# Kernel tuning notes

Measured on AMD Instinct MI355X. Metric: run time of the kernel, lower is better.

The kernel has to match this reference:

```python
import jax, jax.numpy as jnp
import numpy as np

D = 1024
B, S = 4, 2048


def setup_inputs() -> dict:
    key = jax.random.key(0)
    ks = jax.random.split(key, 6)
    sc = 1.0 / np.sqrt(D)  # truncated-normal-ish fan-in scale like hk.Linear default
    return {
        "x": jax.random.normal(ks[0], (B, S, D), dtype=jnp.float32),
        "W_amp1": jax.random.normal(ks[1], (D, D), dtype=jnp.float32) * sc,
        "b_amp1": jnp.zeros((D,), dtype=jnp.float32),
        "W_amp2": jax.random.normal(ks[2], (D, D), dtype=jnp.float32) * sc,
        "b_amp2": jnp.zeros((D,), dtype=jnp.float32),
        "vqc_params": jax.random.uniform(ks[3], (D, 4), dtype=jnp.float32, minval=-np.pi, maxval=np.pi),
        "W_post1": jax.random.normal(ks[4], (D, D), dtype=jnp.float32) * sc,
        "b_post1": jnp.zeros((D,), dtype=jnp.float32),
        "W_post2": jax.random.normal(ks[5], (D, D), dtype=jnp.float32) * sc,
        "b_post2": jnp.zeros((D,), dtype=jnp.float32),
    }


def reference(x, W_amp1, b_amp1, W_amp2, b_amp2, vqc_params,
              W_post1, b_post1, W_post2, b_post2):
    # amplitude encoder: Linear -> tanh -> Linear
    amp = jnp.tanh(x @ W_amp1 + b_amp1) @ W_amp2 + b_amp2  # [B,S,D]

    # variational quantum circuit, vectorized over channels:
    # per-channel i: out_i = amp_i*cos(theta_i/2) + Re(amp_i*sin(theta_i/2)*e^{i phi_i})
    #              = amp_i * (cos(theta_i/2) + sin(theta_i/2)*cos(phi_i))
    theta = vqc_params[:, 0]  # [D]
    phi = vqc_params[:, 1]    # [D]
    scale = jnp.cos(theta * 0.5) + jnp.sin(theta * 0.5) * jnp.cos(phi)  # [D]
    q = amp * scale  # broadcast over [B,S,D]

    # classical post: Linear -> silu -> Linear
    out = jax.nn.silu(q @ W_post1 + b_post1) @ W_post2 + b_post2
    return out
```

## Files before the change

kernel.cpp:

```cpp
#include <hip/hip_runtime.h>
#include <hip/hip_bf16.h>
#include <math.h>

#define DD 1024
#define MM 8192

typedef __attribute__((ext_vector_type(8))) short short8;
typedef __attribute__((ext_vector_type(4))) float f32x4;

__device__ inline unsigned short f32_to_bf16(float f) {
  union { float f; unsigned u; } v; v.f = f;
  unsigned u = v.u;
  u += 0x7FFFu + ((u >> 16) & 1u);
  return (unsigned short)(u >> 16);
}

__global__ void k_convert_x(const float4* __restrict__ x, ushort4* __restrict__ o, int n4) {
  int i = blockIdx.x * blockDim.x + threadIdx.x;
  int stride = gridDim.x * blockDim.x;
  for (; i < n4; i += stride) {
    float4 v = x[i];
    ushort4 r;
    r.x = f32_to_bf16(v.x); r.y = f32_to_bf16(v.y);
    r.z = f32_to_bf16(v.z); r.w = f32_to_bf16(v.w);
    o[i] = r;
  }
}

__global__ void k_transpose_w(const float* __restrict__ w0, const float* __restrict__ w1,
                              const float* __restrict__ w2, const float* __restrict__ w3,
                              unsigned short* __restrict__ o0, unsigned short* __restrict__ o1,
                              unsigned short* __restrict__ o2, unsigned short* __restrict__ o3) {
  const float* src; unsigned short* dst;
  switch (blockIdx.z) {
    case 0: src = w0; dst = o0; break;
    case 1: src = w1; dst = o1; break;
    case 2: src = w2; dst = o2; break;
    default: src = w3; dst = o3; break;
  }
  __shared__ float t[32][33];
  int tx = threadIdx.x, ty = threadIdx.y;
  int c0 = blockIdx.x * 32, r0 = blockIdx.y * 32;
  #pragma unroll
  for (int i = 0; i < 4; i++)
    t[ty + 8 * i][tx] = src[(size_t)(r0 + ty + 8 * i) * DD + c0 + tx];
  __syncthreads();
  #pragma unroll
  for (int i = 0; i < 4; i++)
    dst[(size_t)(c0 + ty + 8 * i) * DD + r0 + tx] = f32_to_bf16(t[tx][ty + 8 * i]);
}

__global__ void k_scale(const float* __restrict__ vqc, float* __restrict__ sc) {
  int d = blockIdx.x * blockDim.x + threadIdx.x;
  if (d < DD) {
    float th = vqc[d * 4 + 0] * 0.5f, ph = vqc[d * 4 + 1];
    sc[d] = cosf(th) + sinf(th) * cosf(ph);
  }
}

template <int EPI>
__global__ void k_gemm(const unsigned short* __restrict__ A,
                       const unsigned short* __restrict__ Bt,
                       const float* __restrict__ bias,
                       const float* __restrict__ scale,
                       void* __restrict__ Cout) {
  constexpr int K = DD, N = DD;
  __shared__ unsigned short As[128 * 64];
  __shared__ unsigned short Bs[128 * 64];
  const int tid = threadIdx.x;
  const int wave = tid >> 6, lane = tid & 63;
  const int wr = wave >> 1, wc = wave & 1;

  const int L = blockIdx.y * gridDim.x + blockIdx.x;
  const int bx = (L >> 3) & 7;
  const int by = (L & 7) | ((L >> 6) << 3);
  const int rowA0 = by * 128, colB0 = bx * 128;

  const int lr = lane & 15, lk = (lane >> 4) * 8;
  const int srow = lane >> 3;
  const int sswz = ((lane & 7) ^ srow) * 8;

  f32x4 acc[4][4] = {};

  for (int k0 = 0; k0 < K; k0 += 64) {
    #pragma unroll
    for (int i = 0; i < 4; i++) {
      int r = wave * 32 + i * 8;
      const unsigned short* ga = A + (size_t)(rowA0 + r + srow) * K + k0 + sswz;
      __builtin_amdgcn_global_load_lds(
          (const __attribute__((address_space(1))) unsigned int*)ga,
          (__attribute__((address_space(3))) unsigned int*)(As + r * 64), 16, 0, 0);
      const unsigned short* gb = Bt + (size_t)(colB0 + r + srow) * K + k0 + sswz;
      __builtin_amdgcn_global_load_lds(
          (const __attribute__((address_space(1))) unsigned int*)gb,
          (__attribute__((address_space(3))) unsigned int*)(Bs + r * 64), 16, 0, 0);
    }
    __syncthreads();

    #pragma unroll
    for (int kk = 0; kk < 64; kk += 32) {
      short8 a[4], b[4];
      #pragma unroll
      for (int m = 0; m < 4; m++) {
        int row = wr * 64 + m * 16 + lr;
        a[m] = *(const short8*)(As + row * 64 + (((((kk + lk) >> 3)) ^ (row & 7)) << 3));
      }
      #pragma unroll
      for (int n = 0; n < 4; n++) {
        int row = wc * 64 + n * 16 + lr;
        b[n] = *(const short8*)(Bs + row * 64 + (((((kk + lk) >> 3)) ^ (row & 7)) << 3));
      }
      #pragma unroll
      for (int m = 0; m < 4; m++)
        #pragma unroll
        for (int n = 0; n < 4; n++)
          acc[m][n] = __builtin_amdgcn_mfma_f32_16x16x32_bf16(a[m], b[n], acc[m][n], 0, 0, 0);
    }
    __syncthreads();
  }

  const int row0 = rowA0 + wr * 64;
  const int col0 = colB0 + wc * 64;
  #pragma unroll
  for (int n = 0; n < 4; n++) {
    const int col = col0 + n * 16 + lr;
    const float bv = bias[col];
    const float sv = (EPI == 1) ? scale[col] : 0.f;
    #pragma unroll
    for (int m = 0; m < 4; m++) {
      #pragma unroll
      for (int j = 0; j < 4; j++) {
        int row = row0 + m * 16 + (lane >> 4) * 4 + j;
        float z = acc[m][n][j] + bv;
        if constexpr (EPI == 0) {
          ((unsigned short*)Cout)[(size_t)row * N + col] = f32_to_bf16(tanhf(z));
        } else if constexpr (EPI == 1) {
          ((unsigned short*)Cout)[(size_t)row * N + col] = f32_to_bf16(z * sv);
        } else if constexpr (EPI == 2) {
          ((unsigned short*)Cout)[(size_t)row * N + col] = f32_to_bf16(z / (1.f + __expf(-z)));
        } else {
          ((float*)Cout)[(size_t)row * N + col] = z;
        }
      }
    }
  }
}

extern "C" void kernel_launch(void* const* d_in, const int* in_sizes, int n_in,
                              void* d_out, int out_size, void* d_ws, size_t ws_size,
                              hipStream_t stream) {
  const float* x   = (const float*)d_in[0];
  const float* W1  = (const float*)d_in[1];
  const float* b1  = (const float*)d_in[2];
  const float* W2  = (const float*)d_in[3];
  const float* b2  = (const float*)d_in[4];
  const float* vqc = (const float*)d_in[5];
  const float* Wp1 = (const float*)d_in[6];
  const float* bp1 = (const float*)d_in[7];
  const float* Wp2 = (const float*)d_in[8];
  const float* bp2 = (const float*)d_in[9];

  char* ws = (char*)d_ws;
  unsigned short* actA = (unsigned short*)ws;
  unsigned short* actB = (unsigned short*)(ws + (16u << 20));
  unsigned short* Wt0  = (unsigned short*)(ws + (32u << 20));
  unsigned short* Wt1  = (unsigned short*)(ws + (34u << 20));
  unsigned short* Wt2  = (unsigned short*)(ws + (36u << 20));
  unsigned short* Wt3  = (unsigned short*)(ws + (38u << 20));
  float* scale = (float*)(ws + (40u << 20));

  k_convert_x<<<2048, 256, 0, stream>>>((const float4*)x, (ushort4*)actA, MM * DD / 4);
  k_transpose_w<<<dim3(32, 32, 4), dim3(32, 8), 0, stream>>>(W1, W2, Wp1, Wp2, Wt0, Wt1, Wt2, Wt3);
  k_scale<<<4, 256, 0, stream>>>(vqc, scale);

  dim3 g(DD / 128, MM / 128), b(256);
  k_gemm<0><<<g, b, 0, stream>>>(actA, Wt0, b1,  nullptr, actB);
  k_gemm<1><<<g, b, 0, stream>>>(actB, Wt1, b2,  scale,   actA);
  k_gemm<2><<<g, b, 0, stream>>>(actA, Wt2, bp1, nullptr, actB);
  k_gemm<3><<<g, b, 0, stream>>>(actB, Wt3, bp2, nullptr, d_out);
}
```

Measured before the change: 118.8 us.

## Triple-buffer GEMM LDS tiles with 256x128 blocks and 8 waves

Restructures the bf16 MFMA GEMM so each block uses 512 threads and a 256x128 output tile. Global-to-LDS loads are issued two K-steps ahead into a three-stage ring buffer, and the per-step double syncthreads is replaced by a partial vmcnt wait plus barrier. It also raises wave priority around the MFMA burst. The aim is to hide load latency and halve B-tile refetches per output. In exchange it uses more LDS (about 144KB per block), gives up the previous L2-friendly block swizzle, and halves the grid to 256 blocks.

Result: slower. 141.4 us (+19.0%).

```diff
diff --git a/kernel.cpp b/kernel.cpp
--- a/kernel.cpp
+++ b/kernel.cpp
@@ -59,43 +59,62 @@
 }
 
 template <int EPI>
+__launch_bounds__(512, 2)
 __global__ void k_gemm(const unsigned short* __restrict__ A,
                        const unsigned short* __restrict__ Bt,
                        const float* __restrict__ bias,
                        const float* __restrict__ scale,
                        void* __restrict__ Cout) {
   constexpr int K = DD, N = DD;
-  __shared__ unsigned short As[128 * 64];
-  __shared__ unsigned short Bs[128 * 64];
+  constexpr int NT = K / 64;
+  __shared__ unsigned short As[3][256 * 64];
+  __shared__ unsigned short Bs[3][128 * 64];
   const int tid = threadIdx.x;
   const int wave = tid >> 6, lane = tid & 63;
   const int wr = wave >> 1, wc = wave & 1;
 
   const int L = blockIdx.y * gridDim.x + blockIdx.x;
-  const int bx = (L >> 3) & 7;
-  const int by = (L & 7) | ((L >> 6) << 3);
-  const int rowA0 = by * 128, colB0 = bx * 128;
+  const int bx = L & 7, by = L >> 3;
+  const int rowA0 = by * 256, colB0 = bx * 128;
 
   const int lr = lane & 15, lk = (lane >> 4) * 8;
   const int srow = lane >> 3;
   const int sswz = ((lane & 7) ^ srow) * 8;
 
+  const unsigned short* gA[4];
+  const unsigned short* gB[2];
+  #pragma unroll
+  for (int i = 0; i < 4; i++)
+    gA[i] = A + (size_t)(rowA0 + i * 64 + wave * 8 + srow) * K + sswz;
+  #pragma unroll
+  for (int j = 0; j < 2; j++)
+    gB[j] = Bt + (size_t)(colB0 + j * 64 + wave * 8 + srow) * K + sswz;
+
+  auto STAGE = [&](int buf, int t) {
+    const int ko = t * 64;
+    #pragma unroll
+    for (int i = 0; i < 4; i++)
+      __builtin_amdgcn_global_load_lds(
+          (const __attribute__((address_space(1))) unsigned int*)(gA[i] + ko),
+          (__attribute__((address_space(3))) unsigned int*)(&As[buf][(i * 64 + wave * 8) * 64]),
+          16, 0, 0);
+    #pragma unroll
+    for (int j = 0; j < 2; j++)
+      __builtin_amdgcn_global_load_lds(
+          (const __attribute__((address_space(1))) unsigned int*)(gB[j] + ko),
+          (__attribute__((address_space(3))) unsigned int*)(&Bs[buf][(j * 64 + wave * 8) * 64]),
+          16, 0, 0);
+  };
+
   f32x4 acc[4][4] = {};
 
-  for (int k0 = 0; k0 < K; k0 += 64) {
-    #pragma unroll
-    for (int i = 0; i < 4; i++) {
-      int r = wave * 32 + i * 8;
-      const unsigned short* ga = A + (size_t)(rowA0 + r + srow) * K + k0 + sswz;
-      __builtin_amdgcn_global_load_lds(
-          (const __attribute__((address_space(1))) unsigned int*)ga,
-          (__attribute__((address_space(3))) unsigned int*)(As + r * 64), 16, 0, 0);
-      const unsigned short* gb = Bt + (size_t)(colB0 + r + srow) * K + k0 + sswz;
-      __builtin_amdgcn_global_load_lds(
-          (const __attribute__((address_space(1))) unsigned int*)gb,
-          (__attribute__((address_space(3))) unsigned int*)(Bs + r * 64), 16, 0, 0);
-    }
-    __syncthreads();
+  STAGE(0, 0);
+  STAGE(1, 1);
+  asm volatile("s_waitcnt vmcnt(6)\ns_barrier" ::: "memory");
+
+  for (int t = 0; t < NT; ++t) {
+    const int cur = t % 3;
+    if (t + 2 < NT) STAGE((t + 2) % 3, t + 2);
 
     #pragma unroll
     for (int kk = 0; kk < 64; kk += 32) {
@@ -103,20 +122,26 @@
       #pragma unroll
       for (int m = 0; m < 4; m++) {
         int row = wr * 64 + m * 16 + lr;
-        a[m] = *(const short8*)(As + row * 64 + (((((kk + lk) >> 3)) ^ (row & 7)) << 3));
+        a[m] = *(const short8*)(&As[cur][row * 64 + ((((kk + lk) >> 3) ^ (row & 7)) << 3)]);
       }
       #pragma unroll
       for (int n = 0; n < 4; n++) {
         int row = wc * 64 + n * 16 + lr;
-        b[n] = *(const short8*)(Bs + row * 64 + (((((kk + lk) >> 3)) ^ (row & 7)) << 3));
+        b[n] = *(const short8*)(&Bs[cur][row * 64 + ((((kk + lk) >> 3) ^ (row & 7)) << 3)]);
       }
+      __builtin_amdgcn_s_setprio(1);
       #pragma unroll
       for (int m = 0; m < 4; m++)
         #pragma unroll
         for (int n = 0; n < 4; n++)
           acc[m][n] = __builtin_amdgcn_mfma_f32_16x16x32_bf16(a[m], b[n], acc[m][n], 0, 0, 0);
+      __builtin_amdgcn_s_setprio(0);
     }
-    __syncthreads();
+
+    if (t < NT - 1) {
+      if (t + 2 < NT) asm volatile("s_waitcnt vmcnt(6)\ns_barrier" ::: "memory");
+      else            asm volatile("s_waitcnt vmcnt(0)\ns_barrier" ::: "memory");
+    }
   }
 
   const int row0 = rowA0 + wr * 64;
@@ -173,7 +198,7 @@
   k_transpose_w<<<dim3(32, 32, 4), dim3(32, 8), 0, stream>>>(W1, W2, Wp1, Wp2, Wt0, Wt1, Wt2, Wt3);
   k_scale<<<4, 256, 0, stream>>>(vqc, scale);
 
-  dim3 g(DD / 128, MM / 128), b(256);
+  dim3 g(DD / 128, MM / 256), b(512);
   k_gemm<0><<<g, b, 0, stream>>>(actA, Wt0, b1,  nullptr, actB);
   k_gemm<1><<<g, b, 0, stream>>>(actB, Wt1, b2,  scale,   actA);
   k_gemm<2><<<g, b, 0, stream>>>(actA, Wt2, bp1, nullptr, actB);
```

## Merge prep kernels into one launch and shrink GEMM tile to 128x64

Applied to the files above, without the earlier changes.

Folds the x conversion, weight transpose and scale computation into a single prep kernel, which removes two launches. The GEMM block tile shrinks from 128x128 to 128x64, doubling the grid to 1024 blocks so the many CUs get more blocks, and adds launch_bounds(256,4) for higher occupancy. The trade-off is less data reuse per block, so A tiles are reloaded twice as often and the MFMA-to-load ratio drops.

Result: no change. 120.0 us (+1.0%).

```diff
diff --git a/kernel.cpp b/kernel.cpp
--- a/kernel.cpp
+++ b/kernel.cpp
@@ -15,50 +15,57 @@
   return (unsigned short)(u >> 16);
 }
 
-__global__ void k_convert_x(const float4* __restrict__ x, ushort4* __restrict__ o, int n4) {
-  int i = blockIdx.x * blockDim.x + threadIdx.x;
-  int stride = gridDim.x * blockDim.x;
-  for (; i < n4; i += stride) {
-    float4 v = x[i];
-    ushort4 r;
-    r.x = f32_to_bf16(v.x); r.y = f32_to_bf16(v.y);
-    r.z = f32_to_bf16(v.z); r.w = f32_to_bf16(v.w);
-    o[i] = r;
-  }
-}
-
-__global__ void k_transpose_w(const float* __restrict__ w0, const float* __restrict__ w1,
-                              const float* __restrict__ w2, const float* __restrict__ w3,
-                              unsigned short* __restrict__ o0, unsigned short* __restrict__ o1,
-                              unsigned short* __restrict__ o2, unsigned short* __restrict__ o3) {
-  const float* src; unsigned short* dst;
-  switch (blockIdx.z) {
-    case 0: src = w0; dst = o0; break;
-    case 1: src = w1; dst = o1; break;
-    case 2: src = w2; dst = o2; break;
-    default: src = w3; dst = o3; break;
-  }
-  __shared__ float t[32][33];
-  int tx = threadIdx.x, ty = threadIdx.y;
-  int c0 = blockIdx.x * 32, r0 = blockIdx.y * 32;
-  #pragma unroll
-  for (int i = 0; i < 4; i++)
-    t[ty + 8 * i][tx] = src[(size_t)(r0 + ty + 8 * i) * DD + c0 + tx];
-  __syncthreads();
-  #pragma unroll
-  for (int i = 0; i < 4; i++)
-    dst[(size_t)(c0 + ty + 8 * i) * DD + r0 + tx] = f32_to_bf16(t[tx][ty + 8 * i]);
-}
-
-__global__ void k_scale(const float* __restrict__ vqc, float* __restrict__ sc) {
-  int d = blockIdx.x * blockDim.x + threadIdx.x;
-  if (d < DD) {
-    float th = vqc[d * 4 + 0] * 0.5f, ph = vqc[d * 4 + 1];
-    sc[d] = cosf(th) + sinf(th) * cosf(ph);
+__global__ void k_prep(const float* __restrict__ x, unsigned short* __restrict__ xb,
+                       const float* __restrict__ w0, const float* __restrict__ w1,
+                       const float* __restrict__ w2, const float* __restrict__ w3,
+                       unsigned short* __restrict__ o0, unsigned short* __restrict__ o1,
+                       unsigned short* __restrict__ o2, unsigned short* __restrict__ o3,
+                       const float* __restrict__ vqc, float* __restrict__ sc) {
+  const int bid = blockIdx.x, tid = threadIdx.x;
+  if (bid < 4096) {
+    const float4* xv = (const float4*)x;
+    ushort4* ov = (ushort4*)xb;
+    int i = bid * 256 + tid;
+    #pragma unroll
+    for (int r = 0; r < 2; r++, i += 4096 * 256) {
+      float4 v = xv[i];
+      ushort4 u;
+      u.x = f32_to_bf16(v.x); u.y = f32_to_bf16(v.y);
+      u.z = f32_to_bf16(v.z); u.w = f32_to_bf16(v.w);
+      ov[i] = u;
+    }
+  } else if (bid < 8192) {
+    const int rel = bid - 4096;
+    const float* src; unsigned short* dst;
+    switch (rel >> 10) {
+      case 0: src = w0; dst = o0; break;
+      case 1: src = w1; dst = o1; break;
+      case 2: src = w2; dst = o2; break;
+      default: src = w3; dst = o3; break;
+    }
+    const int t = rel & 1023;
+    const int r0 = (t >> 5) * 32, c0 = (t & 31) * 32;
+    __shared__ float tl[32][33];
+    const int tx = tid & 31, ty = tid >> 5;
+    #pragma unroll
+    for (int i = 0; i < 4; i++)
+      tl[ty + 8 * i][tx] = src[(size_t)(r0 + ty + 8 * i) * DD + c0 + tx];
+    __syncthreads();
+    #pragma unroll
+    for (int i = 0; i < 4; i++)
+      dst[(size_t)(c0 + ty + 8 * i) * DD + r0 + tx] = f32_to_bf16(tl[tx][ty + 8 * i]);
+  } else {
+    #pragma unroll
+    for (int k = 0; k < 4; k++) {
+      int d = tid + k * 256;
+      float th = vqc[d * 4 + 0] * 0.5f, ph = vqc[d * 4 + 1];
+      sc[d] = cosf(th) + sinf(th) * cosf(ph);
+    }
   }
 }
 
 template <int EPI>
+__launch_bounds__(256, 4)
 __global__ void k_gemm(const unsigned short* __restrict__ A,
                        const unsigned short* __restrict__ Bt,
                        const float* __restrict__ bias,
@@ -66,30 +73,34 @@
                        void* __restrict__ Cout) {
   constexpr int K = DD, N = DD;
   __shared__ unsigned short As[128 * 64];
-  __shared__ unsigned short Bs[128 * 64];
+  __shared__ unsigned short Bs[64 * 64];
   const int tid = threadIdx.x;
   const int wave = tid >> 6, lane = tid & 63;
   const int wr = wave >> 1, wc = wave & 1;
 
   const int L = blockIdx.y * gridDim.x + blockIdx.x;
-  const int bx = (L >> 3) & 7;
-  const int by = (L & 7) | ((L >> 6) << 3);
-  const int rowA0 = by * 128, colB0 = bx * 128;
+  const int bx = (L >> 3) & 15;
+  const int by = (L & 7) | ((L >> 7) << 3);
+  const int rowA0 = by * 128, colB0 = bx * 64;
 
   const int lr = lane & 15, lk = (lane >> 4) * 8;
   const int srow = lane >> 3;
   const int sswz = ((lane & 7) ^ srow) * 8;
 
-  f32x4 acc[4][4] = {};
+  f32x4 acc[4][2] = {};
 
   for (int k0 = 0; k0 < K; k0 += 64) {
     #pragma unroll
     for (int i = 0; i < 4; i++) {
-      int r = wave * 32 + i * 8;
+      int r = i * 32 + wave * 8;
       const unsigned short* ga = A + (size_t)(rowA0 + r + srow) * K + k0 + sswz;
       __builtin_amdgcn_global_load_lds(
           (const __attribute__((address_space(1))) unsigned int*)ga,
           (__attribute__((address_space(3))) unsigned int*)(As + r * 64), 16, 0, 0);
+    }
+    #pragma unroll
+    for (int j = 0; j < 2; j++) {
+      int r = j * 32 + wave * 8;
       const unsigned short* gb = Bt + (size_t)(colB0 + r + srow) * K + k0 + sswz;
       __builtin_amdgcn_global_load_lds(
           (const __attribute__((address_space(1))) unsigned int*)gb,
@@ -99,30 +110,30 @@
 
     #pragma unroll
     for (int kk = 0; kk < 64; kk += 32) {
-      short8 a[4], b[4];
+      short8 a[4], b[2];
       #pragma unroll
       for (int m = 0; m < 4; m++) {
         int row = wr * 64 + m * 16 + lr;
-        a[m] = *(const short8*)(As + row * 64 + (((((kk + lk) >> 3)) ^ (row & 7)) << 3));
+        a[m] = *(const short8*)(As + row * 64 + ((((kk + lk) >> 3) ^ (row & 7)) << 3));
       }
       #pragma unroll
-      for (int n = 0; n < 4; n++) {
-        int row = wc * 64 + n * 16 + lr;
-        b[n] = *(const short8*)(Bs + row * 64 + (((((kk + lk) >> 3)) ^ (row & 7)) << 3));
+      for (int n = 0; n < 2; n++) {
+        int row = wc * 32 + n * 16 + lr;
+        b[n] = *(const short8*)(Bs + row * 64 + ((((kk + lk) >> 3) ^ (row & 7)) << 3));
       }
       #pragma unroll
       for (int m = 0; m < 4; m++)
         #pragma unroll
-        for (int n = 0; n < 4; n++)
+        for (int n = 0; n < 2; n++)
           acc[m][n] = __builtin_amdgcn_mfma_f32_16x16x32_bf16(a[m], b[n], acc[m][n], 0, 0, 0);
     }
     __syncthreads();
   }
 
   const int row0 = rowA0 + wr * 64;
-  const int col0 = colB0 + wc * 64;
+  const int col0 = colB0 + wc * 32;
   #pragma unroll
-  for (int n = 0; n < 4; n++) {
+  for (int n = 0; n < 2; n++) {
     const int col = col0 + n * 16 + lr;
     const float bv = bias[col];
     const float sv = (EPI == 1) ? scale[col] : 0.f;
@@ -169,11 +180,10 @@
   unsigned short* Wt3  = (unsigned short*)(ws + (38u << 20));
   float* scale = (float*)(ws + (40u << 20));
 
-  k_convert_x<<<2048, 256, 0, stream>>>((const float4*)x, (ushort4*)actA, MM * DD / 4);
-  k_transpose_w<<<dim3(32, 32, 4), dim3(32, 8), 0, stream>>>(W1, W2, Wp1, Wp2, Wt0, Wt1, Wt2, Wt3);
-  k_scale<<<4, 256, 0, stream>>>(vqc, scale);
+  k_prep<<<8193, 256, 0, stream>>>(x, actA, W1, W2, Wp1, Wp2,
+                                   Wt0, Wt1, Wt2, Wt3, vqc, scale);
 
-  dim3 g(DD / 128, MM / 128), b(256);
+  dim3 g(DD / 64, MM / 128), b(256);
   k_gemm<0><<<g, b, 0, stream>>>(actA, Wt0, b1,  nullptr, actB);
   k_gemm<1><<<g, b, 0, stream>>>(actB, Wt1, b2,  scale,   actA);
   k_gemm<2><<<g, b, 0, stream>>>(actA, Wt2, bp1, nullptr, actB);
```
